# Kernel tuning notes

Hardware: AMD Instinct MI355X
Metric: run time of the kernel (lower is better)

## Reference

```python
import jax, jax.numpy as jnp
import numpy as np

NUM_HEADS = 8
D_HEAD = 16
RY = RX = 2
PH = 2 * RY + 1
PW = 2 * RX + 1
P = PH * PW  # 25 spatial positions per patch


def setup_inputs() -> dict:
    key = jax.random.key(0)
    ks = jax.random.split(key, 7)
    B, T, H, W, C = 1, 3, 96, 96, 128
    Ck = NUM_HEADS * D_HEAD
    w = lambda k, shp: jax.random.normal(k, shp, jnp.float32) * 0.05
    return {
        "x": jax.random.normal(ks[0], (B, T, H, W, C), jnp.float32),
        "Wq": w(ks[1], (C, Ck)),
        "Wk": w(ks[2], (C, Ck)),
        "Wv": w(ks[3], (C, Ck)),
        "Wo": w(ks[4], (Ck, C)),
        "temp_emb": w(ks[5], (T, Ck)),
        "sp_emb": w(ks[6], (P, Ck)),
    }


def _neighbor_idx(N, r):
    # Edge handling: patch center is clipped into the valid interior, matching
    # extract_patches(VALID) + gather_nd with clipped indices in the original.
    c = jnp.clip(jnp.arange(N), r, N - r - 1)
    return c[:, None] + jnp.arange(-r, r + 1)[None, :]  # (N, 2r+1)


def _query_spatial_idx(H, W):
    # Position of each query pixel inside its (clipped) patch.
    yc = jnp.clip(jnp.arange(H), RY, H - RY - 1)
    xc = jnp.clip(jnp.arange(W), RX, W - RX - 1)
    yr = jnp.arange(H) - yc + RY  # (H,)
    xr = jnp.arange(W) - xc + RX  # (W,)
    return yr[:, None] * PW + xr[None, :]  # (H, W) in [0, P)


def reference(x, Wq, Wk, Wv, Wo, temp_emb, sp_emb):
    B, T, H, W, C = x.shape
    h, d = NUM_HEADS, D_HEAD
    Ck = h * d
    # 1x1 conv projections (no bias) == channel matmuls
    Q = jnp.einsum('bqyxc,ck->bqyxk', x, Wq)
    K = jnp.einsum('bqyxc,ck->bqyxk', x, Wk)
    V = jnp.einsum('bqyxc,ck->bqyxk', x, Wv)
    # positional encodings added AFTER projection (attention space)
    K = K + temp_emb[None, :, None, None, :]
    qidx = _query_spatial_idx(H, W)  # (H, W)
    Q = Q + temp_emb[None, :, None, None, :] + sp_emb[qidx][None, None]
    # local spatial patch extraction with clipped-edge handling
    ynb = _neighbor_idx(H, RY)  # (H, PH)
    xnb = _neighbor_idx(W, RX)  # (W, PW)
    Kp = K[:, :, ynb[:, None, :, None], xnb[None, :, None, :], :]  # (B,T,H,W,PH,PW,Ck)
    Vp = V[:, :, ynb[:, None, :, None], xnb[None, :, None, :], :]
    Kp = Kp.reshape(B, T, H, W, P, Ck) + sp_emb[None, None, None, None]
    Vp = Vp.reshape(B, T, H, W, P, Ck)
    # merge key time into the neighborhood axis: (B,H,W,T*P,h,d)
    Kn = Kp.transpose(0, 2, 3, 1, 4, 5).reshape(B, H, W, T * P, h, d)
    Vn = Vp.transpose(0, 2, 3, 1, 4, 5).reshape(B, H, W, T * P, h, d)
    Qh = Q.reshape(B, T, H, W, h, d)
    scale = 1.0 / jnp.sqrt(jnp.asarray(d, x.dtype))
    scores = jnp.einsum('bqyxnd,byxknd->bqyxnk', Qh, Kn) * scale
    attn = jax.nn.softmax(scores, axis=-1)  # over T*P neighborhood
    out = jnp.einsum('bqyxnk,byxknd->bqyxnd', attn, Vn).reshape(B, T, H, W, Ck)
    out = jnp.einsum('bqyxk,kc->bqyxc', out, Wo)  # output 1x1 conv
    # return_list=False -> concatenate the T outputs along channels
    return out.transpose(0, 2, 3, 1, 4).reshape(B, H, W, T * C)
```

## Files before the change

### kernel.cpp

```cpp
#include <hip/hip_runtime.h>
#include <hip/hip_bf16.h>
#include <math.h>

#define TT 3
#define HH 96
#define WWD 96
#define CCH 128
#define NROWS (TT*HH*WWD)

typedef __attribute__((ext_vector_type(8))) short short8;
typedef __attribute__((ext_vector_type(4))) short short4v;
typedef __attribute__((ext_vector_type(4))) float float4v;

__device__ __forceinline__ float bfu(unsigned short u){ union{unsigned u;float f;}c; c.u=((unsigned)u)<<16; return c.f; }
__device__ __forceinline__ unsigned short f2bf(float f){ __hip_bfloat16 h=__float2bfloat16(f); return *(unsigned short*)&h; }

#if defined(__has_builtin)
#if __has_builtin(__builtin_amdgcn_mfma_f32_16x16x16bf16_1k)
#define MFMA16(A,B,C) __builtin_amdgcn_mfma_f32_16x16x16bf16_1k(A,B,C,0,0,0)
#endif
#endif
#ifndef MFMA16
static __device__ __forceinline__ float4v mfma16_asm(short4v a, short4v b, float4v c){
    float4v d;
    asm("v_mfma_f32_16x16x16_bf16 %0, %1, %2, %3" : "=v"(d) : "v"(a), "v"(b), "v"(c));
    return d;
}
#define MFMA16(A,B,C) mfma16_asm(A,B,C)
#endif

#define QSCL 0.36067376022224085f

__launch_bounds__(256)
__global__ void prep_kernel(const float* __restrict__ Wq, const float* __restrict__ Wk,
                            const float* __restrict__ Wv, const float* __restrict__ Wo,
                            unsigned short* __restrict__ Wt, unsigned short* __restrict__ Wo1,
                            unsigned short* __restrict__ Wo2) {
    __shared__ float ts[32][33];
    const int m = blockIdx.x >> 4, tile = blockIdx.x & 15;
    const int k0 = (tile >> 2) * 32, n0 = (tile & 3) * 32;
    const float* src = (m == 0) ? Wq : (m == 1) ? Wk : (m == 2) ? Wv : Wo;
    const int tid = threadIdx.x;
    const int c = tid & 31, r8 = tid >> 5;
#pragma unroll
    for (int rr = 0; rr < 4; ++rr) {
        int r = r8 * 4 + rr;
        ts[r][c] = src[(size_t)(k0 + r) * 128 + n0 + c];
    }
    __syncthreads();
#pragma unroll
    for (int rr = 0; rr < 4; ++rr) {
        int r = r8 * 4 + rr;
        float v = ts[c][r];
        if (m < 3) {
            Wt[(size_t)(m * 128 + n0 + r) * 128 + k0 + c] = f2bf(v);
        } else {
            unsigned short w1 = f2bf(v);
            Wo1[(size_t)(n0 + r) * 128 + k0 + c] = w1;
            Wo2[(size_t)(n0 + r) * 128 + k0 + c] = f2bf(v - bfu(w1));
        }
    }
}

__launch_bounds__(512)
__global__ void qkv_kernel(const float* __restrict__ x,
                           const unsigned short* __restrict__ Wt,
                           const float* __restrict__ temp_emb,
                           const float* __restrict__ sp_emb,
                           unsigned short* __restrict__ Qb,
                           unsigned short* __restrict__ Kb,
                           unsigned short* __restrict__ Vb) {
    __shared__ __align__(16) char smem[33792];
    unsigned short* xs = (unsigned short*)smem;
    float* OF          = (float*)smem;

    const int tid = threadIdx.x;
    const int q0 = blockIdx.x * 64;
    const int t = q0 / (HH * WWD);

    for (int e = tid; e < 2048; e += 512) {
        int row = e >> 5, col = (e & 31) * 4;
        float4 v = *(const float4*)(x + (size_t)(q0 + row) * CCH + col);
        ushort4 u; u.x = f2bf(v.x); u.y = f2bf(v.y); u.z = f2bf(v.z); u.w = f2bf(v.w);
        *(ushort4*)&xs[row * 136 + col] = u;
    }
    __syncthreads();

    const int w = tid >> 6, lane = tid & 63, quad = lane >> 4, l16 = lane & 15;

    float4v acc[3][4];
#pragma unroll
    for (int m = 0; m < 3; ++m)
#pragma unroll
        for (int nt = 0; nt < 4; ++nt) acc[m][nt] = (float4v){0,0,0,0};

#pragma unroll
    for (int ks = 0; ks < 4; ++ks) {
        short8 b[4];
#pragma unroll
        for (int nt = 0; nt < 4; ++nt)
            b[nt] = *(const short8*)&xs[(nt * 16 + l16) * 136 + ks * 32 + quad * 8];
#pragma unroll
        for (int m = 0; m < 3; ++m) {
            short8 a = *(const short8*)(Wt + (size_t)(m * 128 + w * 16 + l16) * CCH + ks * 32 + quad * 8);
#pragma unroll
            for (int nt = 0; nt < 4; ++nt)
                acc[m][nt] = __builtin_amdgcn_mfma_f32_16x16x32_bf16(a, b[nt], acc[m][nt], 0, 0, 0);
        }
    }

    unsigned short* dst[3] = {Qb, Kb, Vb};
#pragma unroll
    for (int m = 0; m < 3; ++m) {
        __syncthreads();
#pragma unroll
        for (int nt = 0; nt < 4; ++nt) {
            float4v a = acc[m][nt];
            float4 o; o.x = a[0]; o.y = a[1]; o.z = a[2]; o.w = a[3];
            *(float4*)&OF[(nt * 16 + l16) * 132 + w * 16 + quad * 4] = o;
        }
        __syncthreads();
        for (int e = tid; e < 2048; e += 512) {
            int row = e >> 5, c4 = (e & 31);
            int ch = c4 * 4;
            float4 v = *(const float4*)&OF[row * 132 + ch];
            int q = q0 + row;
            ushort4 u;
            if (m == 0) {
                int rem = q - t * (HH * WWD);
                int yy = rem / WWD, xx = rem - (rem / WWD) * WWD;
                int qidx = (yy - min(max(yy, 2), 93) + 2) * 5 + (xx - min(max(xx, 2), 93) + 2);
                float4 te = *(const float4*)(temp_emb + t * CCH + ch);
                float4 se = *(const float4*)(sp_emb + qidx * CCH + ch);
                u.x = f2bf((v.x + te.x + se.x) * QSCL);
                u.y = f2bf((v.y + te.y + se.y) * QSCL);
                u.z = f2bf((v.z + te.z + se.z) * QSCL);
                u.w = f2bf((v.w + te.w + se.w) * QSCL);
            } else if (m == 1) {
                float4 te = *(const float4*)(temp_emb + t * CCH + ch);
                u.x = f2bf(v.x + te.x); u.y = f2bf(v.y + te.y);
                u.z = f2bf(v.z + te.z); u.w = f2bf(v.w + te.w);
            } else {
                u.x = f2bf(v.x); u.y = f2bf(v.y); u.z = f2bf(v.z); u.w = f2bf(v.w);
            }
            *(ushort4*)(dst[m] + (size_t)q * CCH + ch) = u;
        }
    }
}

#define PX 4
#define WIN 8

__launch_bounds__(512, 4)
__global__ void attn_kernel(const unsigned short* __restrict__ Qb,
                            const unsigned short* __restrict__ Kb,
                            const unsigned short* __restrict__ Vb,
                            const float* __restrict__ sp_emb,
                            const unsigned short* __restrict__ Wo1,
                            const unsigned short* __restrict__ Wo2,
                            float* __restrict__ out) {
    __shared__ __align__(16) char smem[75616];
    unsigned short* Ks = (unsigned short*)smem;
    unsigned short* Vt = (unsigned short*)(smem + 17408);
    float* biasL       = (float*)(smem + 34816);
    unsigned short* Os = (unsigned short*)smem;
    float* OF          = (float*)(smem + 34816);

    const int tid = threadIdx.x;
    const int lane = tid & 63;
    const int w = tid >> 6;
    const int quad = lane >> 4, l16 = lane & 15;
    const int h16 = w * 16;

    const int wg = (blockIdx.x & 7) * (576 / 8) + (blockIdx.x >> 3);
    const int bx = wg % (WWD / PX);
    const int by = wg / (WWD / PX);
    const int x0 = bx * PX, y0 = by * PX;
    const int xlo = min(max(x0 - 2, 0), WWD - WIN);
    const int ylo = min(max(y0 - 2, 0), HH - WIN);

    const int qdy = l16 >> 2, qdx = l16 & 3;
    const int yy = y0 + qdy, xx = x0 + qdx;
    const int yc = min(max(yy, 2), HH - 3), xc = min(max(xx, 2), WWD - 3);

    short4v qfr[3];
#pragma unroll
    for (int qt = 0; qt < 3; ++qt) {
        int qrow = qt * (HH * WWD) + yy * WWD + xx;
        qfr[qt] = *(const short4v*)(Qb + (size_t)qrow * CCH + h16 + quad * 4);
    }

    short4v sph[2], spl[2];
#pragma unroll
    for (int tile = 0; tile < 2; ++tile) {
        int kcr = min(tile * 16 + l16, 24);
        float4 v = *(const float4*)(sp_emb + (size_t)kcr * CCH + h16 + quad * 4);
        float vv[4] = {v.x, v.y, v.z, v.w};
        union { short4v s4; unsigned short u[4]; } ph, pl;
#pragma unroll
        for (int i = 0; i < 4; ++i) {
            ph.u[i] = f2bf(vv[i]);
            pl.u[i] = f2bf(vv[i] - bfu(ph.u[i]));
        }
        sph[tile] = ph.s4; spl[tile] = pl.s4;
    }

    const int bbase = w * (3 * 25 * 17);
#pragma unroll
    for (int qt = 0; qt < 3; ++qt) {
#pragma unroll
        for (int tile = 0; tile < 2; ++tile) {
            float4v d = MFMA16(spl[tile], qfr[qt], ((float4v){0.f,0.f,0.f,0.f}));
            d = MFMA16(sph[tile], qfr[qt], d);
#pragma unroll
            for (int r = 0; r < 4; ++r) {
                int kc = tile * 16 + quad * 4 + r;
                if (kc < 25) biasL[bbase + (qt * 25 + kc) * 17 + l16] = d[r];
            }
        }
    }

    int badr[16];
#pragma unroll
    for (int kt = 0; kt < 4; ++kt)
#pragma unroll
        for (int r = 0; r < 4; ++r) {
            int slot = kt * 16 + quad * 4 + r;
            int gy = ylo + (slot >> 3), gx = xlo + (slot & 7);
            int py = gy - yc + 2, px = gx - xc + 2;
            bool ok = (py >= 0) && (py < 5) && (px >= 0) && (px < 5);
            badr[kt * 4 + r] = ok ? (bbase + (py * 5 + px) * 17 + l16) : -1;
        }

    float m[3] = {-1e30f, -1e30f, -1e30f};
    float l[3] = {0.f, 0.f, 0.f};
    float4v oacc[3];
#pragma unroll
    for (int qt = 0; qt < 3; ++qt) oacc[qt] = (float4v){0.f,0.f,0.f,0.f};

    for (int t = 0; t < TT; ++t) {
        __syncthreads();
        for (int e = tid; e < 1024; e += 512) {
            int slot = e >> 4, c = e & 15;
            int gy = ylo + (slot >> 3), gx = xlo + (slot & 7);
            size_t g = ((size_t)(t * HH + gy) * WWD + gx) * CCH + c * 8;
            *(uint4*)&Ks[slot * 136 + c * 8] = *(const uint4*)(Kb + g);
        }
        for (int p = tid; p < 1024; p += 512) {
            int sp2 = p & 31, cq = p >> 5;
            int slot0 = sp2 * 2, ch0 = cq * 4;
            int gy = ylo + (slot0 >> 3), gx = xlo + (slot0 & 7);
            size_t g = ((size_t)(t * HH + gy) * WWD + gx) * CCH + ch0;
            uint2 a = *(const uint2*)(Vb + g);
            uint2 b = *(const uint2*)(Vb + g + CCH);
            unsigned v0 = (a.x & 0xffffu) | (b.x << 16);
            unsigned v1 = (a.x >> 16)     | (b.x & 0xffff0000u);
            unsigned v2 = (a.y & 0xffffu) | (b.y << 16);
            unsigned v3 = (a.y >> 16)     | (b.y & 0xffff0000u);
            *(unsigned*)&Vt[(ch0 + 0) * 68 + slot0] = v0;
            *(unsigned*)&Vt[(ch0 + 1) * 68 + slot0] = v1;
            *(unsigned*)&Vt[(ch0 + 2) * 68 + slot0] = v2;
            *(unsigned*)&Vt[(ch0 + 3) * 68 + slot0] = v3;
        }
        __syncthreads();

        short4v kfr[4], vfr[4];
#pragma unroll
        for (int kt = 0; kt < 4; ++kt) {
            kfr[kt] = *(const short4v*)&Ks[(kt * 16 + l16) * 136 + h16 + quad * 4];
            vfr[kt] = *(const short4v*)&Vt[(h16 + l16) * 68 + kt * 16 + quad * 4];
        }

#pragma unroll
        for (int qt = 0; qt < 3; ++qt) {
            float4v s[4];
#pragma unroll
            for (int kt = 0; kt < 4; ++kt) {
                float4v c;
#pragma unroll
                for (int r = 0; r < 4; ++r) {
                    int a = badr[kt * 4 + r];
                    c[r] = (a < 0) ? -1e30f : biasL[a + qt * 425];
                }
                s[kt] = MFMA16(kfr[kt], qfr[qt], c);
            }
            float mx = m[qt];
#pragma unroll
            for (int kt = 0; kt < 4; ++kt)
#pragma unroll
                for (int r = 0; r < 4; ++r) mx = fmaxf(mx, s[kt][r]);
            mx = fmaxf(mx, __shfl_xor(mx, 16));
            mx = fmaxf(mx, __shfl_xor(mx, 32));
            float corr = exp2f(m[qt] - mx);
            m[qt] = mx;
            l[qt] *= corr;
            float4v oc = oacc[qt] * corr;
            float lsum = 0.f;
            short4v pfr[4];
#pragma unroll
            for (int kt = 0; kt < 4; ++kt) {
                float p0 = exp2f(s[kt][0] - mx), p1 = exp2f(s[kt][1] - mx);
                float p2 = exp2f(s[kt][2] - mx), p3 = exp2f(s[kt][3] - mx);
                lsum += (p0 + p1) + (p2 + p3);
                union { short4v s4; unsigned short u[4]; } pk;
                pk.u[0] = f2bf(p0); pk.u[1] = f2bf(p1);
                pk.u[2] = f2bf(p2); pk.u[3] = f2bf(p3);
                pfr[kt] = pk.s4;
            }
            l[qt] += lsum;
#pragma unroll
            for (int kt = 0; kt < 4; ++kt) oc = MFMA16(vfr[kt], pfr[kt], oc);
            oacc[qt] = oc;
        }
    }

    __syncthreads();
#pragma unroll
    for (int qt = 0; qt < 3; ++qt) {
        float lt = l[qt];
        lt += __shfl_xor(lt, 16);
        lt += __shfl_xor(lt, 32);
        float inv = 1.f / lt;
        union { ushort4 u4; unsigned short u[4]; } ob;
#pragma unroll
        for (int r = 0; r < 4; ++r) ob.u[r] = f2bf(oacc[qt][r] * inv);
        *(ushort4*)&Os[(qt * 16 + l16) * 136 + h16 + quad * 4] = ob.u4;
    }
    __syncthreads();

    float4v pacc[3];
#pragma unroll
    for (int nt = 0; nt < 3; ++nt) pacc[nt] = (float4v){0.f, 0.f, 0.f, 0.f};
#pragma unroll
    for (int ks = 0; ks < 4; ++ks) {
        short8 bfrag[3];
#pragma unroll
        for (int nt = 0; nt < 3; ++nt)
            bfrag[nt] = *(const short8*)&Os[(nt * 16 + l16) * 136 + ks * 32 + quad * 8];
        size_t wo = (size_t)(w * 16 + l16) * CCH + ks * 32 + quad * 8;
        short8 a1 = *(const short8*)(Wo1 + wo);
        short8 a2 = *(const short8*)(Wo2 + wo);
#pragma unroll
        for (int nt = 0; nt < 3; ++nt) {
            pacc[nt] = __builtin_amdgcn_mfma_f32_16x16x32_bf16(a1, bfrag[nt], pacc[nt], 0, 0, 0);
            pacc[nt] = __builtin_amdgcn_mfma_f32_16x16x32_bf16(a2, bfrag[nt], pacc[nt], 0, 0, 0);
        }
    }
#pragma unroll
    for (int nt = 0; nt < 3; ++nt) {
        float4v a = pacc[nt];
        float4 o; o.x = a[0]; o.y = a[1]; o.z = a[2]; o.w = a[3];
        *(float4*)&OF[(nt * 16 + l16) * 132 + w * 16 + quad * 4] = o;
    }
    __syncthreads();

    for (int i = tid; i < 1536; i += 512) {
        int cy = i / 384;
        int r  = i - cy * 384;
        int row12 = r >> 5;
        int ch    = (r & 31) * 4;
        int cx = row12 / 3, nt = row12 - cx * 3;
        float4 v = *(const float4*)&OF[(nt * 16 + cy * 4 + cx) * 132 + ch];
        size_t g = ((size_t)((y0 + cy) * WWD + x0) * TT) * CCH + r * 4;
        *(float4*)(out + g) = v;
    }
}

extern "C" void kernel_launch(void* const* d_in, const int* in_sizes, int n_in,
                              void* d_out, int out_size, void* d_ws, size_t ws_size,
                              hipStream_t stream) {
    const float* x        = (const float*)d_in[0];
    const float* Wq       = (const float*)d_in[1];
    const float* Wk       = (const float*)d_in[2];
    const float* Wv       = (const float*)d_in[3];
    const float* Wo       = (const float*)d_in[4];
    const float* temp_emb = (const float*)d_in[5];
    const float* sp_emb   = (const float*)d_in[6];
    float* out = (float*)d_out;

    const size_t nb = (size_t)NROWS * CCH * 2;
    unsigned short* Qb  = (unsigned short*)d_ws;
    unsigned short* Kb  = (unsigned short*)((char*)d_ws + nb);
    unsigned short* Vb  = (unsigned short*)((char*)d_ws + 2 * nb);
    unsigned short* Wt  = (unsigned short*)((char*)d_ws + 3 * nb);
    unsigned short* Wo1 = Wt + 384 * 128;
    unsigned short* Wo2 = Wo1 + 128 * 128;

    prep_kernel<<<64, 256, 0, stream>>>(Wq, Wk, Wv, Wo, Wt, Wo1, Wo2);
    qkv_kernel<<<NROWS / 64, 512, 0, stream>>>(x, Wt, temp_emb, sp_emb, Qb, Kb, Vb);
    attn_kernel<<<(HH / PX) * (WWD / PX), 512, 0, stream>>>(Qb, Kb, Vb, sp_emb, Wo1, Wo2, out);
}
```

Before: 131.2 us.

## Stage all three time frames of K/V into LDS upfront, drop per-frame barriers

Loads the K and transposed V tiles for all three frames into shared memory at kernel start, overlapping with the Q and bias setup, and replaces the per-frame load/sync loop with a single barrier. This removes two barriers per frame and lets global loads for all frames be in flight together. In exchange LDS use roughly doubles to about 145 KB, and launch bounds drop from 4 to 2 blocks per CU, which lowers occupancy.

```diff
diff --git a/kernel.cpp b/kernel.cpp
--- a/kernel.cpp
+++ b/kernel.cpp
@@ -150,8 +150,10 @@
 
 #define PX 4
 #define WIN 8
-
-__launch_bounds__(512, 4)
+#define KTS 8704
+#define VTS 8704
+
+__launch_bounds__(512, 2)
 __global__ void attn_kernel(const unsigned short* __restrict__ Qb,
                             const unsigned short* __restrict__ Kb,
                             const unsigned short* __restrict__ Vb,
@@ -159,12 +161,12 @@
                             const unsigned short* __restrict__ Wo1,
                             const unsigned short* __restrict__ Wo2,
                             float* __restrict__ out) {
-    __shared__ __align__(16) char smem[75616];
+    __shared__ __align__(16) char smem[145248];
     unsigned short* Ks = (unsigned short*)smem;
-    unsigned short* Vt = (unsigned short*)(smem + 17408);
-    float* biasL       = (float*)(smem + 34816);
+    unsigned short* Vt = (unsigned short*)(smem + 52224);
+    float* biasL       = (float*)(smem + 104448);
     unsigned short* Os = (unsigned short*)smem;
-    float* OF          = (float*)(smem + 34816);
+    float* OF          = (float*)(smem + 52224);
 
     const int tid = threadIdx.x;
     const int lane = tid & 63;
@@ -183,6 +185,36 @@
     const int yy = y0 + qdy, xx = x0 + qdx;
     const int yc = min(max(yy, 2), HH - 3), xc = min(max(xx, 2), WWD - 3);
 
+#pragma unroll
+    for (int i = 0; i < 6; ++i) {
+        int e = i * 512 + tid;
+        int t = e >> 10, r = e & 1023;
+        int slot = r >> 4, c = r & 15;
+        int gy = ylo + (slot >> 3), gx = xlo + (slot & 7);
+        size_t g = ((size_t)(t * HH + gy) * WWD + gx) * CCH + c * 8;
+        *(uint4*)&Ks[t * KTS + slot * 136 + c * 8] = *(const uint4*)(Kb + g);
+    }
+#pragma unroll
+    for (int i = 0; i < 6; ++i) {
+        int p = i * 512 + tid;
+        int t = p >> 10, r = p & 1023;
+        int sp2 = r & 31, cq = r >> 5;
+        int slot0 = sp2 * 2, ch0 = cq * 4;
+        int gy = ylo + (slot0 >> 3), gx = xlo + (slot0 & 7);
+        size_t g = ((size_t)(t * HH + gy) * WWD + gx) * CCH + ch0;
+        uint2 a = *(const uint2*)(Vb + g);
+        uint2 b = *(const uint2*)(Vb + g + CCH);
+        unsigned v0 = (a.x & 0xffffu) | (b.x << 16);
+        unsigned v1 = (a.x >> 16)     | (b.x & 0xffff0000u);
+        unsigned v2 = (a.y & 0xffffu) | (b.y << 16);
+        unsigned v3 = (a.y >> 16)     | (b.y & 0xffff0000u);
+        unsigned short* vt = Vt + t * VTS;
+        *(unsigned*)&vt[(ch0 + 0) * 68 + slot0] = v0;
+        *(unsigned*)&vt[(ch0 + 1) * 68 + slot0] = v1;
+        *(unsigned*)&vt[(ch0 + 2) * 68 + slot0] = v2;
+        *(unsigned*)&vt[(ch0 + 3) * 68 + slot0] = v3;
+    }
+
     short4v qfr[3];
 #pragma unroll
     for (int qt = 0; qt < 3; ++qt) {
@@ -232,43 +264,24 @@
             badr[kt * 4 + r] = ok ? (bbase + (py * 5 + px) * 17 + l16) : -1;
         }
 
+    __syncthreads();
+
     float m[3] = {-1e30f, -1e30f, -1e30f};
     float l[3] = {0.f, 0.f, 0.f};
     float4v oacc[3];
 #pragma unroll
     for (int qt = 0; qt < 3; ++qt) oacc[qt] = (float4v){0.f,0.f,0.f,0.f};
 
+#pragma unroll
     for (int t = 0; t < TT; ++t) {
-        __syncthreads();
-        for (int e = tid; e < 1024; e += 512) {
-            int slot = e >> 4, c = e & 15;
-            int gy = ylo + (slot >> 3), gx = xlo + (slot & 7);
-            size_t g = ((size_t)(t * HH + gy) * WWD + gx) * CCH + c * 8;
-            *(uint4*)&Ks[slot * 136 + c * 8] = *(const uint4*)(Kb + g);
-        }
-        for (int p = tid; p < 1024; p += 512) {
-            int sp2 = p & 31, cq = p >> 5;
-            int slot0 = sp2 * 2, ch0 = cq * 4;
-            int gy = ylo + (slot0 >> 3), gx = xlo + (slot0 & 7);
-            size_t g = ((size_t)(t * HH + gy) * WWD + gx) * CCH + ch0;
-            uint2 a = *(const uint2*)(Vb + g);
-            uint2 b = *(const uint2*)(Vb + g + CCH);
-            unsigned v0 = (a.x & 0xffffu) | (b.x << 16);
-            unsigned v1 = (a.x >> 16)     | (b.x & 0xffff0000u);
-            unsigned v2 = (a.y & 0xffffu) | (b.y << 16);
-            unsigned v3 = (a.y >> 16)     | (b.y & 0xffff0000u);
-            *(unsigned*)&Vt[(ch0 + 0) * 68 + slot0] = v0;
-            *(unsigned*)&Vt[(ch0 + 1) * 68 + slot0] = v1;
-            *(unsigned*)&Vt[(ch0 + 2) * 68 + slot0] = v2;
-            *(unsigned*)&Vt[(ch0 + 3) * 68 + slot0] = v3;
-        }
-        __syncthreads();
+        const unsigned short* Kc = Ks + t * KTS;
+        const unsigned short* Vc = Vt + t * VTS;
 
         short4v kfr[4], vfr[4];
 #pragma unroll
         for (int kt = 0; kt < 4; ++kt) {
-            kfr[kt] = *(const short4v*)&Ks[(kt * 16 + l16) * 136 + h16 + quad * 4];
-            vfr[kt] = *(const short4v*)&Vt[(h16 + l16) * 68 + kt * 16 + quad * 4];
+            kfr[kt] = *(const short4v*)&Kc[(kt * 16 + l16) * 136 + h16 + quad * 4];
+            vfr[kt] = *(const short4v*)&Vc[(h16 + l16) * 68 + kt * 16 + quad * 4];
         }
 
 #pragma unroll
```

After: 142.8 us. 8.8% more time.
